# Kernel tuning notes

Measured on AMD Instinct MI355X. Metric: run time of the kernel, lower is better.

## Reference

```python
import jax, jax.numpy as jnp
import numpy as np

B, T, E, H = 256, 256, 384, 64  # batch, seq (== block_size), embed_dim, head_size

def setup_inputs() -> dict:
    key = jax.random.key(0)
    kx, kq, kk, kv = jax.random.split(key, 4)
    scale = 1.0 / np.sqrt(E)
    return {
        "x": jax.random.normal(kx, (B, T, E), dtype=jnp.float32),
        "Wq": jax.random.normal(kq, (E, H), dtype=jnp.float32) * scale,
        "Wk": jax.random.normal(kk, (E, H), dtype=jnp.float32) * scale,
        "Wv": jax.random.normal(kv, (E, H), dtype=jnp.float32) * scale,
    }

def reference(x, Wq, Wk, Wv):
    # Linear projections (bias-free), faithful to nn.Linear(embed_dim, head_size, bias=False)
    q = jnp.einsum("bte,eh->bth", x, Wq)
    k = jnp.einsum("bte,eh->bth", x, Wk)
    v = jnp.einsum("bte,eh->bth", x, Wv)
    # Scaled QK^T with causal mask, softmax, weighted sum.
    # Dropout is identity in eval mode (reference is deterministic).
    wei = jnp.einsum("bth,bsh->bts", q, k) * (H ** -0.5)  # [B, T, T]
    causal = jnp.tril(jnp.ones((T, T), dtype=bool))
    wei = jnp.where(causal, wei, -jnp.inf)
    wei = jax.nn.softmax(wei, axis=-1)
    out = jnp.einsum("bts,bsh->bth", wei, v)  # [B, T, H]
    return out
```

## Files before the change

kernel.cpp:

```cpp
#include <hip/hip_runtime.h>
#include <hip/hip_bf16.h>

typedef __attribute__((ext_vector_type(8))) short short8;
typedef __attribute__((ext_vector_type(4))) float f32x4;

#define MFMA(a, b, c) __builtin_amdgcn_mfma_f32_16x16x32_bf16((a), (b), (c), 0, 0, 0)

__device__ __forceinline__ unsigned int f2bf2(float a, float b) {
  __hip_bfloat162 h2 = __float22bfloat162_rn(make_float2(a, b));
  union { __hip_bfloat162 h; unsigned int u; } cv; cv.h = h2;
  return cv.u;
}

__device__ __forceinline__ unsigned short f2bf(float f) {
  union { float f; unsigned int u; } v; v.f = f;
  unsigned int u = v.u;
  unsigned int r = u + 0x7FFFu + ((u >> 16) & 1u);
  return (unsigned short)(r >> 16);
}

__global__ void wconv_kernel(const float* __restrict__ Wq, const float* __restrict__ Wk,
                             const float* __restrict__ Wv, unsigned short* __restrict__ W3t) {
  int j = blockIdx.x * 128 + threadIdx.x;
  int s = j / 768;
  int r = j - s * 768;
  int ct = r >> 6, l = r & 63, g = l >> 4, q = l & 15;
  const float* src = (ct < 4) ? Wq : ((ct < 8) ? Wk : Wv);
  int col = 16 * (ct & 3) + q;
  int k = 32 * s + 8 * g;
  float e[8];
#pragma unroll
  for (int i = 0; i < 8; ++i) e[i] = src[(k + i) * 64 + col];
  uint4 u;
  u.x = f2bf2(e[0], e[1]); u.y = f2bf2(e[2], e[3]);
  u.z = f2bf2(e[4], e[5]); u.w = f2bf2(e[6], e[7]);
  *(uint4*)&W3t[j * 8] = u;
}

__global__ __launch_bounds__(1024) void fused_kernel(
    const float* __restrict__ x, const unsigned short* __restrict__ W3t,
    float* __restrict__ out) {
  extern __shared__ unsigned short sm[];
  unsigned short* Ql = sm;
  unsigned short* Kl = sm + 18432;
  unsigned short* Vl = sm + 36864;

  const int tid = threadIdx.x;
  const int w = tid >> 6, lane = tid & 63, g = lane >> 4, q = lane & 15;
  const int b = blockIdx.x;
  const float* xb = x + (long)b * 98304;

#pragma unroll
  for (int i = 0; i < 9; ++i) {
    int idx = tid + i * 1024;
    *(uint4*)&sm[idx * 8] = *(const uint4*)&W3t[idx * 8];
  }

  f32x4 acc[12];
  const f32x4 zf = {0.f, 0.f, 0.f, 0.f};
#pragma unroll
  for (int j = 0; j < 12; ++j) acc[j] = zf;

  const float* xrow = xb + (16 * w + q) * 384 + 8 * g;
  float4 xa[4], xc[4];
#pragma unroll
  for (int i = 0; i < 4; ++i) {
    xa[i] = *(const float4*)&xrow[32 * i];
    xc[i] = *(const float4*)&xrow[32 * i + 4];
  }

  __syncthreads();

#pragma unroll
  for (int ks = 0; ks < 12; ++ks) {
    const int cur = ks & 3;
    uint4 au;
    au.x = f2bf2(xa[cur].x, xa[cur].y); au.y = f2bf2(xa[cur].z, xa[cur].w);
    au.z = f2bf2(xc[cur].x, xc[cur].y); au.w = f2bf2(xc[cur].z, xc[cur].w);
    union { uint4 u; short8 s8; } av; av.u = au;
    if (ks < 8) {
      xa[cur] = *(const float4*)&xrow[32 * (ks + 4)];
      xc[cur] = *(const float4*)&xrow[32 * (ks + 4) + 4];
    }
    const unsigned short* wbase = sm + ks * 6144 + lane * 8;
#pragma unroll
    for (int ct = 0; ct < 12; ++ct) {
      short8 bfr = *(const short8*)&wbase[ct * 512];
      acc[ct] = MFMA(av.s8, bfr, acc[ct]);
    }
  }
  __syncthreads();

  {
    const int mb = 16 * w + 4 * g;
#pragma unroll
    for (int ct = 0; ct < 12; ++ct) {
      int c = 16 * ct + q;
      unsigned int p01 = f2bf2(acc[ct][0], acc[ct][1]);
      unsigned int p23 = f2bf2(acc[ct][2], acc[ct][3]);
      unsigned short h0 = (unsigned short)p01, h1 = (unsigned short)(p01 >> 16);
      unsigned short h2 = (unsigned short)p23, h3 = (unsigned short)(p23 >> 16);
      if (ct < 4) {
        Ql[(mb + 0) * 72 + c] = h0; Ql[(mb + 1) * 72 + c] = h1;
        Ql[(mb + 2) * 72 + c] = h2; Ql[(mb + 3) * 72 + c] = h3;
      } else if (ct < 8) {
        int cc = c - 64;
        Kl[(mb + 0) * 72 + cc] = h0; Kl[(mb + 1) * 72 + cc] = h1;
        Kl[(mb + 2) * 72 + cc] = h2; Kl[(mb + 3) * 72 + cc] = h3;
      } else {
        int hh = c - 128;
        uint2 pk; pk.x = p01; pk.y = p23;
        *(uint2*)&Vl[hh * 264 + mb] = pk;
      }
    }
  }
  __syncthreads();

  unsigned short* Pb = sm + 53760 + w * 640;
  const float SCL = 0.125f * 1.4426950408889634f;
  const int t = w;

  short8 aq0 = *(const short8*)&Ql[(16 * t + q) * 72 + g * 8];
  short8 aq1 = *(const short8*)&Ql[(16 * t + q) * 72 + 32 + g * 8];

  f32x4 o[4];
#pragma unroll
  for (int ct = 0; ct < 4; ++ct) o[ct] = zf;
  float m = -1e30f;
  float lsum = 0.f;

  const int KS = (t >> 1) + 1;
  for (int ks = 0; ks < KS; ++ks) {
    const int j0 = 2 * ks, j1 = 2 * ks + 1;
    const bool has1 = (j1 <= t);
    short8 ka0 = *(const short8*)&Kl[(16 * j0 + q) * 72 + g * 8];
    short8 ka1 = *(const short8*)&Kl[(16 * j0 + q) * 72 + 32 + g * 8];
    f32x4 s0 = MFMA(ka0, aq0, zf);
    s0 = MFMA(ka1, aq1, s0);
    f32x4 s1 = zf;
    if (has1) {
      short8 kb0 = *(const short8*)&Kl[(16 * j1 + q) * 72 + g * 8];
      short8 kb1 = *(const short8*)&Kl[(16 * j1 + q) * 72 + 32 + g * 8];
      s1 = MFMA(kb0, aq0, zf);
      s1 = MFMA(kb1, aq1, s1);
    }
    float v[8];
#pragma unroll
    for (int jr = 0; jr < 4; ++jr) {
      float aa = s0[jr] * SCL;
      if (j0 == t && 4 * g + jr > q) aa = -1e30f;
      v[jr] = aa;
      float c = has1 ? s1[jr] * SCL : -1e30f;
      if (has1 && j1 == t && 4 * g + jr > q) c = -1e30f;
      v[4 + jr] = c;
    }
    float mloc = fmaxf(fmaxf(fmaxf(v[0], v[1]), fmaxf(v[2], v[3])),
                       fmaxf(fmaxf(v[4], v[5]), fmaxf(v[6], v[7])));
    mloc = fmaxf(mloc, __shfl_xor(mloc, 16));
    mloc = fmaxf(mloc, __shfl_xor(mloc, 32));
    float mnew = fmaxf(m, mloc);
    float f = exp2f(m - mnew);
    m = mnew;
    float p[8];
    float ls = 0.f;
#pragma unroll
    for (int i = 0; i < 8; ++i) { p[i] = exp2f(v[i] - mnew); ls += p[i]; }
    lsum = lsum * f + ls;
#pragma unroll
    for (int jr = 0; jr < 4; ++jr) {
      float fr = __shfl(f, 4 * g + jr);
      o[0][jr] *= fr; o[1][jr] *= fr; o[2][jr] *= fr; o[3][jr] *= fr;
    }
    uint2 pa; pa.x = f2bf2(p[0], p[1]); pa.y = f2bf2(p[2], p[3]);
    *(uint2*)&Pb[q * 40 + 4 * g] = pa;
    uint2 pc; pc.x = f2bf2(p[4], p[5]); pc.y = f2bf2(p[6], p[7]);
    *(uint2*)&Pb[q * 40 + 16 + 4 * g] = pc;
    short8 ap = *(const short8*)&Pb[q * 40 + g * 8];
#pragma unroll
    for (int ct = 0; ct < 4; ++ct) {
      short8 bv = *(const short8*)&Vl[(16 * ct + q) * 264 + ks * 32 + g * 8];
      o[ct] = MFMA(ap, bv, o[ct]);
    }
  }

  lsum += __shfl_xor(lsum, 16);
  lsum += __shfl_xor(lsum, 32);
  float linv[4];
#pragma unroll
  for (int jr = 0; jr < 4; ++jr) linv[jr] = 1.0f / __shfl(lsum, 4 * g + jr);

  const long rowbase = (long)b * 256 + 16 * t;
#pragma unroll
  for (int jr = 0; jr < 4; ++jr) {
#pragma unroll
    for (int ct = 0; ct < 4; ++ct) {
      out[(rowbase + 4 * g + jr) * 64 + 16 * ct + q] = o[ct][jr] * linv[jr];
    }
  }
}

extern "C" void kernel_launch(void* const* d_in, const int* in_sizes, int n_in,
                              void* d_out, int out_size, void* d_ws, size_t ws_size,
                              hipStream_t stream) {
  const float* x  = (const float*)d_in[0];
  const float* Wq = (const float*)d_in[1];
  const float* Wk = (const float*)d_in[2];
  const float* Wv = (const float*)d_in[3];
  float* out = (float*)d_out;

  unsigned short* W3t = (unsigned short*)d_ws;

  hipFuncSetAttribute((const void*)fused_kernel,
                      hipFuncAttributeMaxDynamicSharedMemorySize, 147456);

  wconv_kernel<<<72, 128, 0, stream>>>(Wq, Wk, Wv, W3t);
  fused_kernel<<<256, 1024, 147456, stream>>>(x, W3t, out);
}
```

Before: 37.91 us.

## Split QKV projection K-dimension across wave halves with two row tiles per wave

Each wave now computes two 16-row tiles over half of the embedding dimension, so every weight fragment loaded from LDS feeds two MFMAs. The two halves of the block then reduce their partial accumulators through shared memory (stored as bf16) before writing Q/K/V. This halves the LDS weight reads per MFMA but adds an extra reduction pass, two more barriers, more accumulator registers, and an extra bf16 rounding of the partial sums.

Result: slower. 49.37 us (+30.2%).

```diff
diff --git a/kernel.cpp b/kernel.cpp
--- a/kernel.cpp
+++ b/kernel.cpp
@@ -12,11 +12,11 @@
   return cv.u;
 }
 
-__device__ __forceinline__ unsigned short f2bf(float f) {
-  union { float f; unsigned int u; } v; v.f = f;
-  unsigned int u = v.u;
-  unsigned int r = u + 0x7FFFu + ((u >> 16) & 1u);
-  return (unsigned short)(r >> 16);
+__device__ __forceinline__ float bfhi2f(unsigned int u) {
+  union { unsigned int u; float f; } c; c.u = u & 0xffff0000u; return c.f;
+}
+__device__ __forceinline__ float bflo2f(unsigned int u) {
+  union { unsigned int u; float f; } c; c.u = u << 16; return c.f;
 }
 
 __global__ void wconv_kernel(const float* __restrict__ Wq, const float* __restrict__ Wk,
@@ -47,6 +47,8 @@
 
   const int tid = threadIdx.x;
   const int w = tid >> 6, lane = tid & 63, g = lane >> 4, q = lane & 15;
+  const int half = w >> 3;
+  const int wr = w & 7;
   const int b = blockIdx.x;
   const float* xb = x + (long)b * 98304;
 
@@ -56,61 +58,102 @@
     *(uint4*)&sm[idx * 8] = *(const uint4*)&W3t[idx * 8];
   }
 
-  f32x4 acc[12];
+  f32x4 acc0[12], acc1[12];
   const f32x4 zf = {0.f, 0.f, 0.f, 0.f};
 #pragma unroll
-  for (int j = 0; j < 12; ++j) acc[j] = zf;
-
-  const float* xrow = xb + (16 * w + q) * 384 + 8 * g;
-  float4 xa[4], xc[4];
-#pragma unroll
-  for (int i = 0; i < 4; ++i) {
-    xa[i] = *(const float4*)&xrow[32 * i];
-    xc[i] = *(const float4*)&xrow[32 * i + 4];
-  }
-
-  __syncthreads();
-
-#pragma unroll
-  for (int ks = 0; ks < 12; ++ks) {
-    const int cur = ks & 3;
-    uint4 au;
-    au.x = f2bf2(xa[cur].x, xa[cur].y); au.y = f2bf2(xa[cur].z, xa[cur].w);
-    au.z = f2bf2(xc[cur].x, xc[cur].y); au.w = f2bf2(xc[cur].z, xc[cur].w);
-    union { uint4 u; short8 s8; } av; av.u = au;
-    if (ks < 8) {
-      xa[cur] = *(const float4*)&xrow[32 * (ks + 4)];
-      xc[cur] = *(const float4*)&xrow[32 * (ks + 4) + 4];
-    }
-    const unsigned short* wbase = sm + ks * 6144 + lane * 8;
+  for (int j = 0; j < 12; ++j) { acc0[j] = zf; acc1[j] = zf; }
+
+  const float* xrA = xb + (32 * wr + q) * 384 + 192 * half + 8 * g;
+  const float* xrB = xrA + 16 * 384;
+  float4 A0[2], A1[2], B0[2], B1[2];
+#pragma unroll
+  for (int p = 0; p < 2; ++p) {
+    A0[p] = *(const float4*)&xrA[32 * p];
+    A1[p] = *(const float4*)&xrA[32 * p + 4];
+    B0[p] = *(const float4*)&xrB[32 * p];
+    B1[p] = *(const float4*)&xrB[32 * p + 4];
+  }
+
+  __syncthreads();
+
+#pragma unroll
+  for (int ks = 0; ks < 6; ++ks) {
+    const int p = ks & 1;
+    uint4 auA, auB;
+    auA.x = f2bf2(A0[p].x, A0[p].y); auA.y = f2bf2(A0[p].z, A0[p].w);
+    auA.z = f2bf2(A1[p].x, A1[p].y); auA.w = f2bf2(A1[p].z, A1[p].w);
+    auB.x = f2bf2(B0[p].x, B0[p].y); auB.y = f2bf2(B0[p].z, B0[p].w);
+    auB.z = f2bf2(B1[p].x, B1[p].y); auB.w = f2bf2(B1[p].z, B1[p].w);
+    union { uint4 u; short8 s8; } avA, avB;
+    avA.u = auA; avB.u = auB;
+    if (ks < 4) {
+      A0[p] = *(const float4*)&xrA[32 * (ks + 2)];
+      A1[p] = *(const float4*)&xrA[32 * (ks + 2) + 4];
+      B0[p] = *(const float4*)&xrB[32 * (ks + 2)];
+      B1[p] = *(const float4*)&xrB[32 * (ks + 2) + 4];
+    }
+    const unsigned short* wbase = sm + (6 * half + ks) * 6144 + lane * 8;
 #pragma unroll
     for (int ct = 0; ct < 12; ++ct) {
       short8 bfr = *(const short8*)&wbase[ct * 512];
-      acc[ct] = MFMA(av.s8, bfr, acc[ct]);
-    }
-  }
-  __syncthreads();
-
-  {
-    const int mb = 16 * w + 4 * g;
-#pragma unroll
-    for (int ct = 0; ct < 12; ++ct) {
-      int c = 16 * ct + q;
-      unsigned int p01 = f2bf2(acc[ct][0], acc[ct][1]);
-      unsigned int p23 = f2bf2(acc[ct][2], acc[ct][3]);
-      unsigned short h0 = (unsigned short)p01, h1 = (unsigned short)(p01 >> 16);
-      unsigned short h2 = (unsigned short)p23, h3 = (unsigned short)(p23 >> 16);
-      if (ct < 4) {
-        Ql[(mb + 0) * 72 + c] = h0; Ql[(mb + 1) * 72 + c] = h1;
-        Ql[(mb + 2) * 72 + c] = h2; Ql[(mb + 3) * 72 + c] = h3;
-      } else if (ct < 8) {
-        int cc = c - 64;
-        Kl[(mb + 0) * 72 + cc] = h0; Kl[(mb + 1) * 72 + cc] = h1;
-        Kl[(mb + 2) * 72 + cc] = h2; Kl[(mb + 3) * 72 + cc] = h3;
-      } else {
-        int hh = c - 128;
-        uint2 pk; pk.x = p01; pk.y = p23;
-        *(uint2*)&Vl[hh * 264 + mb] = pk;
+      acc0[ct] = MFMA(avA.s8, bfr, acc0[ct]);
+      acc1[ct] = MFMA(avB.s8, bfr, acc1[ct]);
+    }
+  }
+  __syncthreads();
+
+  if (half == 1) {
+#pragma unroll
+    for (int rt = 0; rt < 2; ++rt) {
+#pragma unroll
+      for (int ct = 0; ct < 12; ++ct) {
+        const f32x4 a = rt ? acc1[ct] : acc0[ct];
+        uint2 pk;
+        pk.x = f2bf2(a[0], a[1]);
+        pk.y = f2bf2(a[2], a[3]);
+        *(uint2*)&sm[((wr * 24 + rt * 12 + ct) * 64 + lane) * 4] = pk;
+      }
+    }
+  }
+  __syncthreads();
+  if (half == 0) {
+#pragma unroll
+    for (int rt = 0; rt < 2; ++rt) {
+#pragma unroll
+      for (int ct = 0; ct < 12; ++ct) {
+        uint2 pk = *(const uint2*)&sm[((wr * 24 + rt * 12 + ct) * 64 + lane) * 4];
+        f32x4& a = rt ? acc1[ct] : acc0[ct];
+        a[0] += bflo2f(pk.x); a[1] += bfhi2f(pk.x);
+        a[2] += bflo2f(pk.y); a[3] += bfhi2f(pk.y);
+      }
+    }
+  }
+  __syncthreads();
+
+  if (half == 0) {
+#pragma unroll
+    for (int rt = 0; rt < 2; ++rt) {
+      const int mb = 32 * wr + 16 * rt + 4 * g;
+#pragma unroll
+      for (int ct = 0; ct < 12; ++ct) {
+        const f32x4 a = rt ? acc1[ct] : acc0[ct];
+        int c = 16 * ct + q;
+        unsigned int p01 = f2bf2(a[0], a[1]);
+        unsigned int p23 = f2bf2(a[2], a[3]);
+        unsigned short h0 = (unsigned short)p01, h1 = (unsigned short)(p01 >> 16);
+        unsigned short h2 = (unsigned short)p23, h3 = (unsigned short)(p23 >> 16);
+        if (ct < 4) {
+          Ql[(mb + 0) * 72 + c] = h0; Ql[(mb + 1) * 72 + c] = h1;
+          Ql[(mb + 2) * 72 + c] = h2; Ql[(mb + 3) * 72 + c] = h3;
+        } else if (ct < 8) {
+          int cc = c - 64;
+          Kl[(mb + 0) * 72 + cc] = h0; Kl[(mb + 1) * 72 + cc] = h1;
+          Kl[(mb + 2) * 72 + cc] = h2; Kl[(mb + 3) * 72 + cc] = h3;
+        } else {
+          int hh = c - 128;
+          uint2 pk; pk.x = p01; pk.y = p23;
+          *(uint2*)&Vl[hh * 264 + mb] = pk;
+        }
       }
     }
   }
```

## Use 32x32 MFMA for QKV projection and balance causal tiles across 512-thread blocks

Applied to the files above, without the earlier changes.

Halves the block to 8 waves. Each wave now computes a 32-row QKV projection tile with 32x32x16 bf16 MFMAs, and the weight layout in the conversion kernel is reordered to match. In the attention phase each wave processes a pair of query tiles (w and 15-w) to balance the triangular causal work. This is meant to raise operand reuse per weight LDS read and to remove load imbalance between waves. The cost is fewer waves per block to hide latency, more accumulator registers, and the x prefetch depth drops from four stages to one.

Result: slower. 39.48 us (+4.2%).

```diff
diff --git a/kernel.cpp b/kernel.cpp
--- a/kernel.cpp
+++ b/kernel.cpp
@@ -3,14 +3,10 @@
 
 typedef __attribute__((ext_vector_type(8))) short short8;
 typedef __attribute__((ext_vector_type(4))) float f32x4;
-
-#define MFMA(a, b, c) __builtin_amdgcn_mfma_f32_16x16x32_bf16((a), (b), (c), 0, 0, 0)
-
-__device__ __forceinline__ unsigned int f2bf2(float a, float b) {
-  __hip_bfloat162 h2 = __float22bfloat162_rn(make_float2(a, b));
-  union { __hip_bfloat162 h; unsigned int u; } cv; cv.h = h2;
-  return cv.u;
-}
+typedef __attribute__((ext_vector_type(16))) float f32x16;
+
+#define MFMA16(a, b, c) __builtin_amdgcn_mfma_f32_16x16x32_bf16((a), (b), (c), 0, 0, 0)
+#define MFMA32(a, b, c) __builtin_amdgcn_mfma_f32_32x32x16_bf16((a), (b), (c), 0, 0, 0)
 
 __device__ __forceinline__ unsigned short f2bf(float f) {
   union { float f; unsigned int u; } v; v.f = f;
@@ -19,25 +15,32 @@
   return (unsigned short)(r >> 16);
 }
 
+__device__ __forceinline__ unsigned int f2bf2(float a, float b) {
+  __hip_bfloat162 h2 = __float22bfloat162_rn(make_float2(a, b));
+  union { __hip_bfloat162 h; unsigned int u; } cv; cv.h = h2;
+  return cv.u;
+}
+
 __global__ void wconv_kernel(const float* __restrict__ Wq, const float* __restrict__ Wk,
                              const float* __restrict__ Wv, unsigned short* __restrict__ W3t) {
   int j = blockIdx.x * 128 + threadIdx.x;
-  int s = j / 768;
-  int r = j - s * 768;
-  int ct = r >> 6, l = r & 63, g = l >> 4, q = l & 15;
-  const float* src = (ct < 4) ? Wq : ((ct < 8) ? Wk : Wv);
-  int col = 16 * (ct & 3) + q;
-  int k = 32 * s + 8 * g;
+  int s2 = j / 384;
+  int r = j - s2 * 384;
+  int c = r >> 6, l = r & 63;
+  int col = 32 * c + (l & 31);
+  int k = 16 * s2 + 8 * (l >> 5);
+  const float* src = (col < 64) ? Wq : ((col < 128) ? Wk : Wv);
+  int sc = col & 63;
   float e[8];
 #pragma unroll
-  for (int i = 0; i < 8; ++i) e[i] = src[(k + i) * 64 + col];
+  for (int i = 0; i < 8; ++i) e[i] = src[(k + i) * 64 + sc];
   uint4 u;
   u.x = f2bf2(e[0], e[1]); u.y = f2bf2(e[2], e[3]);
   u.z = f2bf2(e[4], e[5]); u.w = f2bf2(e[6], e[7]);
   *(uint4*)&W3t[j * 8] = u;
 }
 
-__global__ __launch_bounds__(1024) void fused_kernel(
+__global__ __launch_bounds__(512) void fused_kernel(
     const float* __restrict__ x, const unsigned short* __restrict__ W3t,
     float* __restrict__ out) {
   extern __shared__ unsigned short sm[];
@@ -47,69 +50,82 @@
 
   const int tid = threadIdx.x;
   const int w = tid >> 6, lane = tid & 63, g = lane >> 4, q = lane & 15;
+  const int l31 = lane & 31, h = lane >> 5;
   const int b = blockIdx.x;
   const float* xb = x + (long)b * 98304;
 
 #pragma unroll
-  for (int i = 0; i < 9; ++i) {
-    int idx = tid + i * 1024;
+  for (int i = 0; i < 18; ++i) {
+    int idx = tid + i * 512;
     *(uint4*)&sm[idx * 8] = *(const uint4*)&W3t[idx * 8];
   }
 
-  f32x4 acc[12];
-  const f32x4 zf = {0.f, 0.f, 0.f, 0.f};
-#pragma unroll
-  for (int j = 0; j < 12; ++j) acc[j] = zf;
-
-  const float* xrow = xb + (16 * w + q) * 384 + 8 * g;
-  float4 xa[4], xc[4];
-#pragma unroll
-  for (int i = 0; i < 4; ++i) {
-    xa[i] = *(const float4*)&xrow[32 * i];
-    xc[i] = *(const float4*)&xrow[32 * i + 4];
-  }
+  f32x16 acc[6];
+#pragma unroll
+  for (int j = 0; j < 6; ++j)
+#pragma unroll
+    for (int r = 0; r < 16; ++r) acc[j][r] = 0.f;
+
+  const float* xrow = xb + (32 * w + l31) * 384 + 8 * h;
+  float4 c0 = *(const float4*)&xrow[0];
+  float4 c1 = *(const float4*)&xrow[4];
+  float4 c2 = *(const float4*)&xrow[16];
+  float4 c3 = *(const float4*)&xrow[20];
 
   __syncthreads();
 
 #pragma unroll
   for (int ks = 0; ks < 12; ++ks) {
-    const int cur = ks & 3;
-    uint4 au;
-    au.x = f2bf2(xa[cur].x, xa[cur].y); au.y = f2bf2(xa[cur].z, xa[cur].w);
-    au.z = f2bf2(xc[cur].x, xc[cur].y); au.w = f2bf2(xc[cur].z, xc[cur].w);
-    union { uint4 u; short8 s8; } av; av.u = au;
-    if (ks < 8) {
-      xa[cur] = *(const float4*)&xrow[32 * (ks + 4)];
-      xc[cur] = *(const float4*)&xrow[32 * (ks + 4) + 4];
-    }
-    const unsigned short* wbase = sm + ks * 6144 + lane * 8;
-#pragma unroll
-    for (int ct = 0; ct < 12; ++ct) {
-      short8 bfr = *(const short8*)&wbase[ct * 512];
-      acc[ct] = MFMA(av.s8, bfr, acc[ct]);
-    }
+    float4 n0, n1, n2, n3;
+    if (ks < 11) {
+      n0 = *(const float4*)&xrow[32 * (ks + 1)];
+      n1 = *(const float4*)&xrow[32 * (ks + 1) + 4];
+      n2 = *(const float4*)&xrow[32 * (ks + 1) + 16];
+      n3 = *(const float4*)&xrow[32 * (ks + 1) + 20];
+    }
+    uint4 a0u, a1u;
+    a0u.x = f2bf2(c0.x, c0.y); a0u.y = f2bf2(c0.z, c0.w);
+    a0u.z = f2bf2(c1.x, c1.y); a0u.w = f2bf2(c1.z, c1.w);
+    a1u.x = f2bf2(c2.x, c2.y); a1u.y = f2bf2(c2.z, c2.w);
+    a1u.z = f2bf2(c3.x, c3.y); a1u.w = f2bf2(c3.z, c3.w);
+    union { uint4 u; short8 s8; } av0, av1;
+    av0.u = a0u; av1.u = a1u;
+    const unsigned short* base = sm + (2 * ks) * 3072 + lane * 8;
+#pragma unroll
+    for (int ct = 0; ct < 6; ++ct) {
+      short8 b0 = *(const short8*)&base[ct * 512];
+      acc[ct] = MFMA32(av0.s8, b0, acc[ct]);
+      short8 b1 = *(const short8*)&base[3072 + ct * 512];
+      acc[ct] = MFMA32(av1.s8, b1, acc[ct]);
+    }
+    if (ks < 11) { c0 = n0; c1 = n1; c2 = n2; c3 = n3; }
   }
   __syncthreads();
 
-  {
-    const int mb = 16 * w + 4 * g;
-#pragma unroll
-    for (int ct = 0; ct < 12; ++ct) {
-      int c = 16 * ct + q;
-      unsigned int p01 = f2bf2(acc[ct][0], acc[ct][1]);
-      unsigned int p23 = f2bf2(acc[ct][2], acc[ct][3]);
-      unsigned short h0 = (unsigned short)p01, h1 = (unsigned short)(p01 >> 16);
-      unsigned short h2 = (unsigned short)p23, h3 = (unsigned short)(p23 >> 16);
-      if (ct < 4) {
-        Ql[(mb + 0) * 72 + c] = h0; Ql[(mb + 1) * 72 + c] = h1;
-        Ql[(mb + 2) * 72 + c] = h2; Ql[(mb + 3) * 72 + c] = h3;
-      } else if (ct < 8) {
-        int cc = c - 64;
-        Kl[(mb + 0) * 72 + cc] = h0; Kl[(mb + 1) * 72 + cc] = h1;
-        Kl[(mb + 2) * 72 + cc] = h2; Kl[(mb + 3) * 72 + cc] = h3;
-      } else {
-        int hh = c - 128;
-        uint2 pk; pk.x = p01; pk.y = p23;
+#pragma unroll
+  for (int ct = 0; ct < 6; ++ct) {
+    const int C = 32 * ct + l31;
+    if (ct < 2) {
+#pragma unroll
+      for (int r = 0; r < 16; ++r) {
+        int row = 32 * w + (r & 3) + 8 * (r >> 2) + 4 * h;
+        Ql[row * 72 + C] = f2bf(acc[ct][r]);
+      }
+    } else if (ct < 4) {
+      const int cc = C - 64;
+#pragma unroll
+      for (int r = 0; r < 16; ++r) {
+        int row = 32 * w + (r & 3) + 8 * (r >> 2) + 4 * h;
+        Kl[row * 72 + cc] = f2bf(acc[ct][r]);
+      }
+    } else {
+      const int hh = C - 128;
+#pragma unroll
+      for (int rq = 0; rq < 4; ++rq) {
+        int mb = 32 * w + 8 * rq + 4 * h;
+        uint2 pk;
+        pk.x = f2bf2(acc[ct][4 * rq + 0], acc[ct][4 * rq + 1]);
+        pk.y = f2bf2(acc[ct][4 * rq + 2], acc[ct][4 * rq + 3]);
         *(uint2*)&Vl[hh * 264 + mb] = pk;
       }
     }
@@ -118,83 +134,88 @@
 
   unsigned short* Pb = sm + 53760 + w * 640;
   const float SCL = 0.125f * 1.4426950408889634f;
-  const int t = w;
-
-  short8 aq0 = *(const short8*)&Ql[(16 * t + q) * 72 + g * 8];
-  short8 aq1 = *(const short8*)&Ql[(16 * t + q) * 72 + 32 + g * 8];
-
-  f32x4 o[4];
-#pragma unroll
-  for (int ct = 0; ct < 4; ++ct) o[ct] = zf;
-  float m = -1e30f;
-  float lsum = 0.f;
-
-  const int KS = (t >> 1) + 1;
-  for (int ks = 0; ks < KS; ++ks) {
-    const int j0 = 2 * ks, j1 = 2 * ks + 1;
-    const bool has1 = (j1 <= t);
-    short8 ka0 = *(const short8*)&Kl[(16 * j0 + q) * 72 + g * 8];
-    short8 ka1 = *(const short8*)&Kl[(16 * j0 + q) * 72 + 32 + g * 8];
-    f32x4 s0 = MFMA(ka0, aq0, zf);
-    s0 = MFMA(ka1, aq1, s0);
-    f32x4 s1 = zf;
-    if (has1) {
-      short8 kb0 = *(const short8*)&Kl[(16 * j1 + q) * 72 + g * 8];
-      short8 kb1 = *(const short8*)&Kl[(16 * j1 + q) * 72 + 32 + g * 8];
-      s1 = MFMA(kb0, aq0, zf);
-      s1 = MFMA(kb1, aq1, s1);
-    }
-    float v[8];
+  const f32x4 zf = {0.f, 0.f, 0.f, 0.f};
+
+#pragma unroll
+  for (int ti = 0; ti < 2; ++ti) {
+    const int t = ti ? (15 - w) : w;
+
+    short8 aq0 = *(const short8*)&Ql[(16 * t + q) * 72 + g * 8];
+    short8 aq1 = *(const short8*)&Ql[(16 * t + q) * 72 + 32 + g * 8];
+
+    f32x4 o[4];
+#pragma unroll
+    for (int ct = 0; ct < 4; ++ct) o[ct] = zf;
+    float m = -1e30f;
+    float lsum = 0.f;
+
+    const int KS = (t >> 1) + 1;
+    for (int ks = 0; ks < KS; ++ks) {
+      const int j0 = 2 * ks, j1 = 2 * ks + 1;
+      const bool has1 = (j1 <= t);
+      short8 ka0 = *(const short8*)&Kl[(16 * j0 + q) * 72 + g * 8];
+      short8 ka1 = *(const short8*)&Kl[(16 * j0 + q) * 72 + 32 + g * 8];
+      f32x4 s0 = MFMA16(ka0, aq0, zf);
+      s0 = MFMA16(ka1, aq1, s0);
+      f32x4 s1 = zf;
+      if (has1) {
+        short8 kb0 = *(const short8*)&Kl[(16 * j1 + q) * 72 + g * 8];
+        short8 kb1 = *(const short8*)&Kl[(16 * j1 + q) * 72 + 32 + g * 8];
+        s1 = MFMA16(kb0, aq0, zf);
+        s1 = MFMA16(kb1, aq1, s1);
+      }
+      float v[8];
+#pragma unroll
+      for (int jr = 0; jr < 4; ++jr) {
+        float aa = s0[jr] * SCL;
+        if (j0 == t && 4 * g + jr > q) aa = -1e30f;
+        v[jr] = aa;
+        float cc = has1 ? s1[jr] * SCL : -1e30f;
+        if (has1 && j1 == t && 4 * g + jr > q) cc = -1e30f;
+        v[4 + jr] = cc;
+      }
+      float mloc = fmaxf(fmaxf(fmaxf(v[0], v[1]), fmaxf(v[2], v[3])),
+                         fmaxf(fmaxf(v[4], v[5]), fmaxf(v[6], v[7])));
+      mloc = fmaxf(mloc, __shfl_xor(mloc, 16));
+      mloc = fmaxf(mloc, __shfl_xor(mloc, 32));
+      float mnew = fmaxf(m, mloc);
+      float f = exp2f(m - mnew);
+      m = mnew;
+      float p[8];
+      float ls = 0.f;
+#pragma unroll
+      for (int i = 0; i < 8; ++i) { p[i] = exp2f(v[i] - mnew); ls += p[i]; }
+      lsum = lsum * f + ls;
+#pragma unroll
+      for (int jr = 0; jr < 4; ++jr) {
+        float fr = __shfl(f, 4 * g + jr);
+        o[0][jr] *= fr; o[1][jr] *= fr; o[2][jr] *= fr; o[3][jr] *= fr;
+      }
+      uint2 pa; pa.x = f2bf2(p[0], p[1]); pa.y = f2bf2(p[2], p[3]);
+      *(uint2*)&Pb[q * 40 + 4 * g] = pa;
+      uint2 pc; pc.x = f2bf2(p[4], p[5]); pc.y = f2bf2(p[6], p[7]);
+      *(uint2*)&Pb[q * 40 + 16 + 4 * g] = pc;
+      short8 ap = *(const short8*)&Pb[q * 40 + g * 8];
+#pragma unroll
+      for (int ct = 0; ct < 4; ++ct) {
+        short8 bv = *(const short8*)&Vl[(16 * ct + q) * 264 + ks * 32 + g * 8];
+        o[ct] = MFMA16(ap, bv, o[ct]);
+      }
+    }
+
+    lsum += __shfl_xor(lsum, 16);
+    lsum += __shfl_xor(lsum, 32);
+    float linv[4];
+#pragma unroll
+    for (int jr = 0; jr < 4; ++jr) linv[jr] = 1.0f / __shfl(lsum, 4 * g + jr);
+
+    const long rowbase = (long)b * 256 + 16 * t;
 #pragma unroll
     for (int jr = 0; jr < 4; ++jr) {
-      float aa = s0[jr] * SCL;
-      if (j0 == t && 4 * g + jr > q) aa = -1e30f;
-      v[jr] = aa;
-      float c = has1 ? s1[jr] * SCL : -1e30f;
-      if (has1 && j1 == t && 4 * g + jr > q) c = -1e30f;
-      v[4 + jr] = c;
-    }
-    float mloc = fmaxf(fmaxf(fmaxf(v[0], v[1]), fmaxf(v[2], v[3])),
-                       fmaxf(fmaxf(v[4], v[5]), fmaxf(v[6], v[7])));
-    mloc = fmaxf(mloc, __shfl_xor(mloc, 16));
-    mloc = fmaxf(mloc, __shfl_xor(mloc, 32));
-    float mnew = fmaxf(m, mloc);
-    float f = exp2f(m - mnew);
-    m = mnew;
-    float p[8];
-    float ls = 0.f;
-#pragma unroll
-    for (int i = 0; i < 8; ++i) { p[i] = exp2f(v[i] - mnew); ls += p[i]; }
-    lsum = lsum * f + ls;
-#pragma unroll
-    for (int jr = 0; jr < 4; ++jr) {
-      float fr = __shfl(f, 4 * g + jr);
-      o[0][jr] *= fr; o[1][jr] *= fr; o[2][jr] *= fr; o[3][jr] *= fr;
-    }
-    uint2 pa; pa.x = f2bf2(p[0], p[1]); pa.y = f2bf2(p[2], p[3]);
-    *(uint2*)&Pb[q * 40 + 4 * g] = pa;
-    uint2 pc; pc.x = f2bf2(p[4], p[5]); pc.y = f2bf2(p[6], p[7]);
-    *(uint2*)&Pb[q * 40 + 16 + 4 * g] = pc;
-    short8 ap = *(const short8*)&Pb[q * 40 + g * 8];
-#pragma unroll
-    for (int ct = 0; ct < 4; ++ct) {
-      short8 bv = *(const short8*)&Vl[(16 * ct + q) * 264 + ks * 32 + g * 8];
-      o[ct] = MFMA(ap, bv, o[ct]);
-    }
-  }
-
-  lsum += __shfl_xor(lsum, 16);
-  lsum += __shfl_xor(lsum, 32);
-  float linv[4];
-#pragma unroll
-  for (int jr = 0; jr < 4; ++jr) linv[jr] = 1.0f / __shfl(lsum, 4 * g + jr);
-
-  const long rowbase = (long)b * 256 + 16 * t;
-#pragma unroll
-  for (int jr = 0; jr < 4; ++jr) {
-#pragma unroll
-    for (int ct = 0; ct < 4; ++ct) {
-      out[(rowbase + 4 * g + jr) * 64 + 16 * ct + q] = o[ct][jr] * linv[jr];
+#pragma unroll
+      for (int ct = 0; ct < 4; ++ct) {
+        out[(rowbase + 4 * g + jr) * 64 + 16 * ct + q] = o[ct][jr] * linv[jr];
+      }
     }
   }
 }
@@ -214,5 +235,5 @@
                       hipFuncAttributeMaxDynamicSharedMemorySize, 147456);
 
   wconv_kernel<<<72, 128, 0, stream>>>(Wq, Wk, Wv, W3t);
-  fused_kernel<<<256, 1024, 147456, stream>>>(x, W3t, out);
-}
+  fused_kernel<<<256, 512, 147456, stream>>>(x, W3t, out);
+}
```
